# Kernel tuning notes

Hardware: AMD Instinct MI355X
Metric: run time of the kernel (lower is better)

Reference implementation:

```python
import jax, jax.numpy as jnp
import numpy as np

MAX_LEN = 20
MIN_LEN = 3


def setup_inputs() -> dict:
    key = jax.random.key(0)
    ks = jax.random.split(key, 7)
    B, latent, hidden, out = 8192, 256, 512, 512
    in_dim = latent + (MAX_LEN - MIN_LEN)  # 273: one-hot length code + noise

    def w(k, shape, fan_in):
        return jax.random.normal(k, shape, jnp.float32) * (1.0 / np.sqrt(fan_in))

    return {
        "x": jax.random.normal(ks[0], (B, latent), jnp.float32),
        "W1": w(ks[1], (hidden, in_dim), in_dim), "b1": jnp.zeros(hidden, jnp.float32),
        "W2": w(ks[2], (hidden, hidden), hidden), "b2": jnp.zeros(hidden, jnp.float32),
        "W3": w(ks[3], (out, hidden), hidden), "b3": jnp.zeros(out, jnp.float32),
        "Wih": w(ks[4], (4 * out, out), out), "Whh": w(ks[5], (4 * out, out), out),
        "bih": jnp.zeros(4 * out, jnp.float32), "bhh": jnp.zeros(4 * out, jnp.float32),
        "sentence_len": 16,
    }


def reference(x, W1, b1, W2, b2, W3, b3, Wih, Whh, bih, bhh, sentence_len):
    B = x.shape[0]
    out = W3.shape[0]
    # length one-hot (deterministic part of forward)
    onehot = jnp.zeros((B, MAX_LEN - MIN_LEN), x.dtype).at[:, MAX_LEN - sentence_len].set(1.0)
    z = jnp.concatenate([onehot, x], axis=1)  # [B, 273]
    h = jax.nn.relu(z @ W1.T + b1)
    h = jax.nn.relu(h @ W2.T + b2)
    x0 = jax.nn.sigmoid(h @ W3.T + b3)  # [B, out] first LSTM input

    bias = bih + bhh
    h0 = jnp.zeros((B, out), x.dtype)
    c0 = jnp.zeros((B, out), x.dtype)

    def step(carry, _):
        inp, h, c = carry
        gates = inp @ Wih.T + h @ Whh.T + bias  # [B, 4*out], torch order i,f,g,o
        i, f, g, o = jnp.split(gates, 4, axis=1)
        c_new = jax.nn.sigmoid(f) * c + jax.nn.sigmoid(i) * jnp.tanh(g)
        h_new = jax.nn.sigmoid(o) * jnp.tanh(c_new)
        # next input is this step's output (the module feeds h_n back in)
        return (h_new, h_new, c_new), h_new

    _, hs = jax.lax.scan(step, (x0, h0, c0), None, length=sentence_len)  # [T, B, out]
    return jnp.transpose(hs, (1, 0, 2))  # [B, T, out]
```

## Files before the change

kernel.cpp:

```cpp
#include <hip/hip_runtime.h>
#include <hip/hip_bf16.h>

typedef __attribute__((ext_vector_type(8))) short s8v;
typedef __attribute__((ext_vector_type(4))) float f4v;

__device__ __forceinline__ void gl_lds16(const void* g, void* l) {
  __builtin_amdgcn_global_load_lds(
      (const __attribute__((address_space(1))) unsigned int*)g,
      (__attribute__((address_space(3))) unsigned int*)l, 16, 0, 0);
}

__device__ __forceinline__ unsigned short f2b(float v) {
  __hip_bfloat16 b = __float2bfloat16(v);
  return __builtin_bit_cast(unsigned short, b);
}

__device__ __forceinline__ float sigm(float x) {
  float e = __builtin_amdgcn_exp2f(-1.442695041f * x);
  return __builtin_amdgcn_rcpf(1.0f + e);
}
__device__ __forceinline__ float tanh_f(float x) {
  float e = __builtin_amdgcn_exp2f(-2.885390082f * x);
  return __builtin_fmaf(2.0f, __builtin_amdgcn_rcpf(1.0f + e), -1.0f);
}


__global__ void k_conv_bf16(const float* __restrict__ src, unsigned short* __restrict__ dst, int n) {
  int i = blockIdx.x * blockDim.x + threadIdx.x;
  if (i < n) dst[i] = f2b(src[i]);
}

__global__ void k_prep_w1(const float* __restrict__ W1, const float* __restrict__ b1,
                          const int* __restrict__ slen,
                          unsigned short* __restrict__ W1x, float* __restrict__ b1e) {
  int i = blockIdx.x * blockDim.x + threadIdx.x;
  if (i < 512 * 256) {
    int n = i >> 8, k = i & 255;
    W1x[i] = f2b(W1[n * 273 + 17 + k]);
  }
  if (i < 512) {
    int col = 20 - *slen;
    b1e[i] = b1[i] + W1[i * 273 + col];
  }
}

__global__ void k_prep_gates(const float* __restrict__ Wih, const float* __restrict__ Whh,
                             const float* __restrict__ bih, const float* __restrict__ bhh,
                             unsigned short* __restrict__ Wihb, unsigned short* __restrict__ Wsum,
                             float* __restrict__ biasg) {
  int i = blockIdx.x * blockDim.x + threadIdx.x;
  if (i < 2048 * 512) {
    float a = Wih[i];
    Wihb[i] = f2b(a);
    Wsum[i] = f2b(a + Whh[i]);
  }
  if (i < 2048) biasg[i] = bih[i] + bhh[i];
}



template <int ACT>
__global__ __launch_bounds__(256)
void k_gemm_bt(const unsigned short* __restrict__ A, const unsigned short* __restrict__ Bt,
               const float* __restrict__ bias, unsigned short* __restrict__ C,
               int M, int N, int K) {
  __shared__ __align__(16) unsigned short As[128 * 32];
  __shared__ __align__(16) unsigned short Bs[128 * 32];
  const int tid = threadIdx.x;
  const int m0 = blockIdx.y * 128, n0 = blockIdx.x * 128;
  const int lane = tid & 63, wave = tid >> 6;
  const int wm = (wave >> 1) * 64, wn = (wave & 1) * 64;
  const int lr = lane & 15, lq = lane >> 4;
  const int sw = (lr >> 1) & 3;
  const int rc = (lq ^ sw) << 3;

  f4v acc[4][4];
#pragma unroll
  for (int i = 0; i < 4; ++i)
#pragma unroll
    for (int j = 0; j < 4; ++j) acc[i][j] = (f4v){0.f, 0.f, 0.f, 0.f};

  for (int k0 = 0; k0 < K; k0 += 32) {
    __syncthreads();
#pragma unroll
    for (int s = 0; s < 2; ++s) {
      int cc = tid + s * 256;
      int row = cc >> 2, c = cc & 3;
      int col = k0 + ((c ^ ((row >> 1) & 3)) << 3);
      gl_lds16(&A[(long)(m0 + row) * K + col], &As[cc * 8]);
      gl_lds16(&Bt[(long)(n0 + row) * K + col], &Bs[cc * 8]);
    }
    __syncthreads();

    s8v a[4], b[4];
#pragma unroll
    for (int i = 0; i < 4; ++i)
      a[i] = *(const s8v*)&As[(wm + i * 16 + lr) * 32 + rc];
#pragma unroll
    for (int j = 0; j < 4; ++j)
      b[j] = *(const s8v*)&Bs[(wn + j * 16 + lr) * 32 + rc];
#pragma unroll
    for (int i = 0; i < 4; ++i)
#pragma unroll
      for (int j = 0; j < 4; ++j)
        acc[i][j] = __builtin_amdgcn_mfma_f32_16x16x32_bf16(a[i], b[j], acc[i][j], 0, 0, 0);
  }

#pragma unroll
  for (int i = 0; i < 4; ++i) {
#pragma unroll
    for (int j = 0; j < 4; ++j) {
#pragma unroll
      for (int r = 0; r < 4; ++r) {
        int m = m0 + wm + i * 16 + lq * 4 + r;
        int n = n0 + wn + j * 16 + lr;
        float v = acc[i][j][r] + bias[n];
        v = (ACT == 0) ? fmaxf(v, 0.0f) : sigm(v);
        C[(long)m * N + n] = f2b(v);
      }
    }
  }
}


__global__ __launch_bounds__(256, 4)
void k_lstm_step4(const unsigned short* __restrict__ A,
                  const unsigned short* __restrict__ Wg,
                  const float* __restrict__ bias,
                  float* __restrict__ Cst,
                  unsigned short* __restrict__ Hout,
                  float* __restrict__ Out,
                  int T, int t, int first) {
  __shared__ __align__(16) unsigned short As[2][128 * 32];
  __shared__ __align__(16) unsigned short Bs[2][4 * 32 * 32];
  const int tid = threadIdx.x;
  const int p = blockIdx.x;
  const int q = p >> 3;
  const int mt = (p & 7) + ((q & 7) << 3);
  const int nt = q >> 3;
  const long m0 = (long)mt * 128;
  const int n0 = nt * 32;
  const int lane = tid & 63, wave = tid >> 6;
  const int lr = lane & 15, lq = lane >> 4;
  const int wr = (wave >> 1) * 64;
  const int wu = (wave & 1) * 16;
  const int rc = ((lq ^ ((lr >> 1) & 3)) << 3);

  f4v acc[4][4];
#pragma unroll
  for (int g = 0; g < 4; ++g)
#pragma unroll
    for (int i = 0; i < 4; ++i) acc[g][i] = (f4v){0.f, 0.f, 0.f, 0.f};

  auto stage = [&](int sel, int kt) {
#pragma unroll
    for (int s = 0; s < 2; ++s) {
      int cc = tid + s * 256;
      int row = cc >> 2, c = cc & 3;
      int col = kt * 32 + ((c ^ ((row >> 1) & 3)) << 3);
      gl_lds16(&A[(m0 + row) * 512 + col], &As[sel][cc * 8]);
    }
#pragma unroll
    for (int s = 0; s < 2; ++s) {
      int cc = tid + s * 256;
      int g = cc >> 7, idx = cc & 127;
      int row = idx >> 2, c = idx & 3;
      int col = kt * 32 + ((c ^ ((row >> 1) & 3)) << 3);
      gl_lds16(&Wg[((long)(g * 512 + n0 + row)) * 512 + col], &Bs[sel][cc * 8]);
    }
  };

  stage(0, 0);
  __syncthreads();

  int sel = 0;
  for (int kt = 0; kt < 16; ++kt) {
    if (kt < 15) stage(sel ^ 1, kt + 1);

    s8v a[4], b[4];
#pragma unroll
    for (int i = 0; i < 4; ++i)
      a[i] = *(const s8v*)&As[sel][(wr + i * 16 + lr) * 32 + rc];
#pragma unroll
    for (int g = 0; g < 4; ++g)
      b[g] = *(const s8v*)&Bs[sel][g * 1024 + (wu + lr) * 32 + rc];
#pragma unroll
    for (int g = 0; g < 4; ++g)
#pragma unroll
      for (int i = 0; i < 4; ++i)
        acc[g][i] = __builtin_amdgcn_mfma_f32_16x16x32_bf16(a[i], b[g], acc[g][i], 0, 0, 0);

    if (kt < 15) {
      __syncthreads();
      sel ^= 1;
    }
  }

  const int u = n0 + wu + lr;
  const float b_i = bias[u];
  const float b_f = bias[512 + u];
  const float b_g = bias[1024 + u];
  const float b_o = bias[1536 + u];
#pragma unroll
  for (int i = 0; i < 4; ++i) {
#pragma unroll
    for (int r = 0; r < 4; ++r) {
      long m = m0 + wr + i * 16 + lq * 4 + r;
      float gi = acc[0][i][r] + b_i;
      float gf = acc[1][i][r] + b_f;
      float gg = acc[2][i][r] + b_g;
      float go = acc[3][i][r] + b_o;
      float c_old = first ? 0.0f : Cst[m * 512 + u];
      float cn = sigm(gf) * c_old + sigm(gi) * tanh_f(gg);
      float h = sigm(go) * tanh_f(cn);
      Cst[m * 512 + u] = cn;
      Hout[m * 512 + u] = f2b(h);
      __builtin_nontemporal_store(h, &Out[(m * T + t) * 512 + u]);
    }
  }
}


extern "C" void kernel_launch(void* const* d_in, const int* in_sizes, int n_in,
                              void* d_out, int out_size, void* d_ws, size_t ws_size,
                              hipStream_t stream) {
  const float* x   = (const float*)d_in[0];
  const float* W1  = (const float*)d_in[1];
  const float* b1  = (const float*)d_in[2];
  const float* W2  = (const float*)d_in[3];
  const float* b2  = (const float*)d_in[4];
  const float* W3  = (const float*)d_in[5];
  const float* b3  = (const float*)d_in[6];
  const float* Wih = (const float*)d_in[7];
  const float* Whh = (const float*)d_in[8];
  const float* bih = (const float*)d_in[9];
  const float* bhh = (const float*)d_in[10];
  const int* slen  = (const int*)d_in[11];
  float* out = (float*)d_out;

  const int B = in_sizes[0] / 256;
  const int T = out_size / (B * 512);

  size_t o = 0;
  auto alloc = [&](size_t bytes) {
    o = (o + 255) & ~(size_t)255;
    void* r = (char*)d_ws + o;
    o += bytes;
    return r;
  };
  unsigned short* xb    = (unsigned short*)alloc((size_t)B * 256 * 2);
  unsigned short* W1x   = (unsigned short*)alloc(512 * 256 * 2);
  unsigned short* W2b   = (unsigned short*)alloc(512 * 512 * 2);
  unsigned short* W3b   = (unsigned short*)alloc(512 * 512 * 2);
  unsigned short* Wihb  = (unsigned short*)alloc(2048 * 512 * 2);
  unsigned short* Wsumb = (unsigned short*)alloc(2048 * 512 * 2);
  float* b1e   = (float*)alloc(512 * 4);
  float* biasg = (float*)alloc(2048 * 4);
  unsigned short* h1 = (unsigned short*)alloc((size_t)B * 512 * 2);
  unsigned short* h2 = (unsigned short*)alloc((size_t)B * 512 * 2);
  float* cbuf = (float*)alloc((size_t)B * 512 * 4);
  (void)ws_size;

  k_conv_bf16<<<(B * 256 + 255) / 256, 256, 0, stream>>>(x, xb, B * 256);
  k_conv_bf16<<<(512 * 512 + 255) / 256, 256, 0, stream>>>(W2, W2b, 512 * 512);
  k_conv_bf16<<<(512 * 512 + 255) / 256, 256, 0, stream>>>(W3, W3b, 512 * 512);
  k_prep_w1<<<(512 * 256 + 255) / 256, 256, 0, stream>>>(W1, b1, slen, W1x, b1e);
  k_prep_gates<<<(2048 * 512 + 255) / 256, 256, 0, stream>>>(Wih, Whh, bih, bhh, Wihb, Wsumb,
                                                             biasg);

  k_gemm_bt<0><<<dim3(4, B / 128), 256, 0, stream>>>(xb, W1x, b1e, h1, B, 512, 256);
  k_gemm_bt<0><<<dim3(4, B / 128), 256, 0, stream>>>(h1, W2b, b2, h2, B, 512, 512);
  k_gemm_bt<1><<<dim3(4, B / 128), 256, 0, stream>>>(h2, W3b, b3, h1, B, 512, 512);

  for (int t = 0; t < T; ++t) {
    const unsigned short* a = (t % 2 == 0) ? h1 : h2;
    unsigned short* ho      = (t % 2 == 0) ? h2 : h1;
    k_lstm_step4<<<dim3(1024), 256, 0, stream>>>(
        a, (t == 0) ? Wihb : Wsumb, biasg, cbuf, ho, out, T, t, (t == 0) ? 1 : 0);
  }
}
```

Baseline: 745.1 us.

## Enlarge LSTM step tile to 256 rows with triple-buffered LDS pipeline

Result: slower. 768.5 us (+3.1%).

```diff
diff --git a/kernel.cpp b/kernel.cpp
--- a/kernel.cpp
+++ b/kernel.cpp
@@ -71,8 +71,7 @@
   const int lane = tid & 63, wave = tid >> 6;
   const int wm = (wave >> 1) * 64, wn = (wave & 1) * 64;
   const int lr = lane & 15, lq = lane >> 4;
-  const int sw = (lr >> 1) & 3;
-  const int rc = (lq ^ sw) << 3;
+  const int rc = ((lq ^ ((lr >> 1) & 3)) << 3);
 
   f4v acc[4][4];
 #pragma unroll
@@ -123,42 +122,44 @@
 }
 
 
-__global__ __launch_bounds__(256, 4)
-void k_lstm_step4(const unsigned short* __restrict__ A,
+__global__ __launch_bounds__(256, 2)
+void k_lstm_step5(const unsigned short* __restrict__ A,
                   const unsigned short* __restrict__ Wg,
                   const float* __restrict__ bias,
                   float* __restrict__ Cst,
                   unsigned short* __restrict__ Hout,
                   float* __restrict__ Out,
                   int T, int t, int first) {
-  __shared__ __align__(16) unsigned short As[2][128 * 32];
-  __shared__ __align__(16) unsigned short Bs[2][4 * 32 * 32];
+  __shared__ __align__(16) unsigned short As[3][256 * 32];
+  __shared__ __align__(16) unsigned short Bs[3][4 * 32 * 32];
   const int tid = threadIdx.x;
   const int p = blockIdx.x;
-  const int q = p >> 3;
-  const int mt = (p & 7) + ((q & 7) << 3);
-  const int nt = q >> 3;
-  const long m0 = (long)mt * 128;
+  const int mt = (p & 7) + (((p >> 3) & 3) << 3);
+  const int nt = p >> 5;
+  const long m0 = (long)mt * 256;
   const int n0 = nt * 32;
   const int lane = tid & 63, wave = tid >> 6;
   const int lr = lane & 15, lq = lane >> 4;
-  const int wr = (wave >> 1) * 64;
-  const int wu = (wave & 1) * 16;
+  const int wr = wave * 64;
   const int rc = ((lq ^ ((lr >> 1) & 3)) << 3);
 
-  f4v acc[4][4];
+  f4v acc[4][4][2];
 #pragma unroll
   for (int g = 0; g < 4; ++g)
 #pragma unroll
-    for (int i = 0; i < 4; ++i) acc[g][i] = (f4v){0.f, 0.f, 0.f, 0.f};
+    for (int i = 0; i < 4; ++i)
+#pragma unroll
+      for (int j = 0; j < 2; ++j) acc[g][i][j] = (f4v){0.f, 0.f, 0.f, 0.f};
 
   auto stage = [&](int sel, int kt) {
-#pragma unroll
-    for (int s = 0; s < 2; ++s) {
+    unsigned short* as = &As[sel][0];
+    unsigned short* bs = &Bs[sel][0];
+#pragma unroll
+    for (int s = 0; s < 4; ++s) {
       int cc = tid + s * 256;
       int row = cc >> 2, c = cc & 3;
       int col = kt * 32 + ((c ^ ((row >> 1) & 3)) << 3);
-      gl_lds16(&A[(m0 + row) * 512 + col], &As[sel][cc * 8]);
+      gl_lds16(&A[(m0 + row) * 512 + col], &as[cc * 8]);
     }
 #pragma unroll
     for (int s = 0; s < 2; ++s) {
@@ -166,56 +167,67 @@
       int g = cc >> 7, idx = cc & 127;
       int row = idx >> 2, c = idx & 3;
       int col = kt * 32 + ((c ^ ((row >> 1) & 3)) << 3);
-      gl_lds16(&Wg[((long)(g * 512 + n0 + row)) * 512 + col], &Bs[sel][cc * 8]);
+      gl_lds16(&Wg[((long)(g * 512 + n0 + row)) * 512 + col], &bs[cc * 8]);
     }
   };
 
   stage(0, 0);
-  __syncthreads();
-
-  int sel = 0;
+  stage(1, 1);
+
+#pragma unroll
   for (int kt = 0; kt < 16; ++kt) {
-    if (kt < 15) stage(sel ^ 1, kt + 1);
-
-    s8v a[4], b[4];
+    if (kt < 15) asm volatile("s_waitcnt vmcnt(6)" ::: "memory");
+    else         asm volatile("s_waitcnt vmcnt(0)" ::: "memory");
+    __builtin_amdgcn_s_barrier();
+    __builtin_amdgcn_sched_barrier(0);
+
+    const int sel = kt % 3;
+    s8v a[4], b[4][2];
 #pragma unroll
     for (int i = 0; i < 4; ++i)
       a[i] = *(const s8v*)&As[sel][(wr + i * 16 + lr) * 32 + rc];
 #pragma unroll
     for (int g = 0; g < 4; ++g)
-      b[g] = *(const s8v*)&Bs[sel][g * 1024 + (wu + lr) * 32 + rc];
+#pragma unroll
+      for (int j = 0; j < 2; ++j)
+        b[g][j] = *(const s8v*)&Bs[sel][g * 1024 + (j * 16 + lr) * 32 + rc];
+
+    if (kt < 14) stage((kt + 2) % 3, kt + 2);
+
+    asm volatile("s_waitcnt lgkmcnt(0)" ::: "memory");
+    __builtin_amdgcn_sched_barrier(0);
 #pragma unroll
     for (int g = 0; g < 4; ++g)
 #pragma unroll
       for (int i = 0; i < 4; ++i)
-        acc[g][i] = __builtin_amdgcn_mfma_f32_16x16x32_bf16(a[i], b[g], acc[g][i], 0, 0, 0);
-
-    if (kt < 15) {
-      __syncthreads();
-      sel ^= 1;
-    }
-  }
-
-  const int u = n0 + wu + lr;
-  const float b_i = bias[u];
-  const float b_f = bias[512 + u];
-  const float b_g = bias[1024 + u];
-  const float b_o = bias[1536 + u];
-#pragma unroll
-  for (int i = 0; i < 4; ++i) {
-#pragma unroll
-    for (int r = 0; r < 4; ++r) {
-      long m = m0 + wr + i * 16 + lq * 4 + r;
-      float gi = acc[0][i][r] + b_i;
-      float gf = acc[1][i][r] + b_f;
-      float gg = acc[2][i][r] + b_g;
-      float go = acc[3][i][r] + b_o;
-      float c_old = first ? 0.0f : Cst[m * 512 + u];
-      float cn = sigm(gf) * c_old + sigm(gi) * tanh_f(gg);
-      float h = sigm(go) * tanh_f(cn);
-      Cst[m * 512 + u] = cn;
-      Hout[m * 512 + u] = f2b(h);
-      __builtin_nontemporal_store(h, &Out[(m * T + t) * 512 + u]);
+#pragma unroll
+        for (int j = 0; j < 2; ++j)
+          acc[g][i][j] = __builtin_amdgcn_mfma_f32_16x16x32_bf16(a[i], b[g][j], acc[g][i][j], 0, 0, 0);
+  }
+
+#pragma unroll
+  for (int j = 0; j < 2; ++j) {
+    const int u = n0 + j * 16 + lr;
+    const float b_i = bias[u];
+    const float b_f = bias[512 + u];
+    const float b_g = bias[1024 + u];
+    const float b_o = bias[1536 + u];
+#pragma unroll
+    for (int i = 0; i < 4; ++i) {
+#pragma unroll
+      for (int r = 0; r < 4; ++r) {
+        long m = m0 + wr + i * 16 + lq * 4 + r;
+        float gi = acc[0][i][j][r] + b_i;
+        float gf = acc[1][i][j][r] + b_f;
+        float gg = acc[2][i][j][r] + b_g;
+        float go = acc[3][i][j][r] + b_o;
+        float c_old = first ? 0.0f : Cst[m * 512 + u];
+        float cn = sigm(gf) * c_old + sigm(gi) * tanh_f(gg);
+        float h = sigm(go) * tanh_f(cn);
+        Cst[m * 512 + u] = cn;
+        Hout[m * 512 + u] = f2b(h);
+        __builtin_nontemporal_store(h, &Out[(m * T + t) * 512 + u]);
+      }
     }
   }
 }
@@ -275,7 +287,7 @@
   for (int t = 0; t < T; ++t) {
     const unsigned short* a = (t % 2 == 0) ? h1 : h2;
     unsigned short* ho      = (t % 2 == 0) ? h2 : h1;
-    k_lstm_step4<<<dim3(1024), 256, 0, stream>>>(
+    k_lstm_step5<<<dim3(512), 256, 0, stream>>>(
         a, (t == 0) ? Wihb : Wsumb, biasg, cbuf, ho, out, T, t, (t == 0) ? 1 : 0);
   }
 }
```
